# Optimization experiments

Measured on AMD Instinct MI355X. Metric: run time of the kernel, lower is better.

Reference implementation:

```python
import jax, jax.numpy as jnp
import numpy as np
import math

B, S, D, DFF, L, H, V = 8, 1024, 768, 3072, 6, 12, 70
DH = D // H


def setup_inputs():
    key = jax.random.key(0)
    ks = jax.random.split(key, 16)
    s = 0.02
    n = lambda k, sh: jax.random.normal(k, sh, dtype=jnp.float32) * s
    return {
        "x": jax.random.randint(ks[0], (B, S), 0, V),
        "mask": jnp.ones((S, S), dtype=jnp.int32),
        "color_W": n(ks[1], (4, 256)),
        "shape_W": n(ks[2], (4, 256)),
        "qty_W": n(ks[3], (4, 256)),
        "special_W": n(ks[4], (6, D)),
        "Wq": n(ks[5], (L, D, D)),
        "Wk": n(ks[6], (L, D, D)),
        "Wv": n(ks[7], (L, D, D)),
        "Wo": n(ks[8], (L, D, D)),
        "bo": jnp.zeros((L, D), jnp.float32),
        "ln1_g": jnp.ones((L, D), jnp.float32),
        "ln1_b": jnp.zeros((L, D), jnp.float32),
        "ln2_g": jnp.ones((L, D), jnp.float32),
        "ln2_b": jnp.zeros((L, D), jnp.float32),
        "W1": n(ks[9], (L, D, DFF)),
        "b1": jnp.zeros((L, DFF), jnp.float32),
        "W2": n(ks[10], (L, DFF, D)),
        "b2": jnp.zeros((L, D), jnp.float32),
        "Wout": n(ks[11], (D, V)),
        "bout": jnp.zeros((V,), jnp.float32),
    }


def _layernorm(x, g, b, eps=1e-5):
    m = x.mean(-1, keepdims=True)
    v = ((x - m) ** 2).mean(-1, keepdims=True)
    return (x - m) / jnp.sqrt(v + eps) * g + b


def _embed(x, color_W, shape_W, qty_W, special_W):
    # feature tokens (<64): color=t//16, shape=(t%16)//4, quantity=t%4
    color = jnp.clip(x // 16, 0, 3)
    shp = (x % 16) // 4
    qty = x % 4
    feat = jnp.concatenate([color_W[color], shape_W[shp], qty_W[qty]], axis=-1)  # [B,S,D]
    spec = special_W[jnp.clip(x - 64, 0, 5)]  # [B,S,D]
    emb = jnp.where((x < 64)[..., None], feat, spec)
    # sinusoidal PE: pe[p,2i]=sin(p/10000^(2i/D)), pe[p,2i+1]=cos(same angle)
    pos = jnp.arange(S, dtype=jnp.float32)[:, None]
    i = jnp.arange(0, D, 2, dtype=jnp.float32)
    ang = pos / jnp.power(10000.0, i / D)  # [S, D/2]
    pe = jnp.zeros((S, D), jnp.float32).at[:, 0::2].set(jnp.sin(ang)).at[:, 1::2].set(jnp.cos(ang))
    return emb * math.sqrt(D) + pe


def reference(x, mask, color_W, shape_W, qty_W, special_W, Wq, Wk, Wv, Wo, bo,
              ln1_g, ln1_b, ln2_g, ln2_b, W1, b1, W2, b2, Wout, bout):
    h = _embed(x, color_W, shape_W, qty_W, special_W)  # [B,S,D]
    neg_mask = (mask == 0)[None, None]  # [1,1,S,S]
    for l in range(L):
        q = (h @ Wq[l]).reshape(B, S, H, DH).transpose(0, 2, 1, 3)
        k = (h @ Wk[l]).reshape(B, S, H, DH).transpose(0, 2, 1, 3)
        v = (h @ Wv[l]).reshape(B, S, H, DH).transpose(0, 2, 1, 3)
        scores = jnp.einsum('bhqd,bhkd->bhqk', q, k) / math.sqrt(DH)
        scores = jnp.where(neg_mask, -1e9, scores)
        w = jax.nn.softmax(scores, axis=-1)
        o = jnp.einsum('bhqk,bhkd->bhqd', w, v).transpose(0, 2, 1, 3).reshape(B, S, D)
        o = o @ Wo[l] + bo[l]
        h = _layernorm(h + o, ln1_g[l], ln1_b[l])
        f = jax.nn.relu(h @ W1[l] + b1[l]) @ W2[l] + b2[l]
        h = _layernorm(h + f, ln2_g[l], ln2_b[l])
    return h @ Wout + bout  # [B,S,V]
```

## Files before the change

kernel.cpp:

```cpp
#include <hip/hip_runtime.h>
#include <hip/hip_bf16.h>

#define B_   8
#define S_   1024
#define D_   768
#define DFF_ 3072
#define L_   6
#define H_   12
#define DH_  64
#define V_   70
#define M_   (B_*S_)

typedef __attribute__((ext_vector_type(4))) float  f32x4;
typedef __attribute__((ext_vector_type(8))) short  s16x8;
typedef __attribute__((ext_vector_type(8))) __bf16 bfv8;
typedef __hip_bfloat16 bf16;

__device__ __forceinline__ float b2f(short u) {
  return __uint_as_float(((unsigned)(unsigned short)u) << 16);
}

__device__ __forceinline__ f32x4 mfma16x16x32(s16x8 a, s16x8 b, f32x4 c) {
  return __builtin_amdgcn_mfma_f32_16x16x32_bf16(
      __builtin_bit_cast(bfv8, a), __builtin_bit_cast(bfv8, b), c, 0, 0, 0);
}

__global__ __launch_bounds__(256)
void embed_kernel(const int* __restrict__ x,
                  const float* __restrict__ cW, const float* __restrict__ sW,
                  const float* __restrict__ qW, const float* __restrict__ spW,
                  float* __restrict__ hf, bf16* __restrict__ hb)
{
  int tok  = blockIdx.x;
  int spos = tok & (S_ - 1);
  int t    = x[tok];
  for (int idx = threadIdx.x; idx < D_; idx += 256) {
    float e;
    if (t < 64) {
      int color = t >> 4;       if (color > 3) color = 3;
      int shp   = (t & 15) >> 2;
      int qty   = t & 3;
      e = (idx < 256) ? cW[color*256 + idx]
        : (idx < 512) ? sW[shp*256 + idx - 256]
                      : qW[qty*256 + idx - 512];
    } else {
      int sp = t - 64; if (sp > 5) sp = 5;
      e = spW[sp*D_ + idx];
    }
    int   i2  = idx & ~1;
    float ang = (float)spos * expf(-logf(10000.f) * (float)i2 / (float)D_);
    float pe  = (idx & 1) ? cosf(ang) : sinf(ang);
    float v   = e * 27.712812921102035f + pe;
    hf[(size_t)tok*D_ + idx] = v;
    hb[(size_t)tok*D_ + idx] = __float2bfloat16(v);
  }
}

__global__ __launch_bounds__(256)
void transpose_kernel(const float* __restrict__ in, bf16* __restrict__ out,
                      int K, int N)
{
  __shared__ __align__(16) float s[64][65];
  int n0 = blockIdx.x * 64, k0 = blockIdx.y * 64;
  int tx = threadIdx.x & 63, ty = threadIdx.x >> 6;
  #pragma unroll
  for (int i = 0; i < 16; i++) {
    int r = i*4 + ty;
    s[r][tx] = in[(size_t)(k0 + r)*N + n0 + tx];
  }
  __syncthreads();
  #pragma unroll
  for (int i = 0; i < 16; i++) {
    int r = i*4 + ty;
    out[(size_t)(n0 + r)*K + k0 + tx] = __float2bfloat16(s[tx][r]);
  }
}

__global__ __launch_bounds__(256)
void vT_kernel(const bf16* __restrict__ v, bf16* __restrict__ vt)
{
  __shared__ short tile[64][68];
  int b = blockIdx.z, h = blockIdx.y, s0 = blockIdx.x*64;
  int tr = threadIdx.x >> 4, tc4 = (threadIdx.x & 15)*4;
  #pragma unroll
  for (int i = 0; i < 4; i++) {
    int row = i*16 + tr;
    short4 w = *(const short4*)((const short*)v + (size_t)(b*S_ + s0 + row)*D_ + h*DH_ + tc4);
    tile[row][tc4+0]=w.x; tile[row][tc4+1]=w.y; tile[row][tc4+2]=w.z; tile[row][tc4+3]=w.w;
  }
  __syncthreads();
  #pragma unroll
  for (int i = 0; i < 4; i++) {
    int d = i*16 + tr;
    short4 o2;
    o2.x = tile[tc4+0][d]; o2.y = tile[tc4+1][d]; o2.z = tile[tc4+2][d]; o2.w = tile[tc4+3][d];
    *(short4*)((short*)vt + ((size_t)(b*H_ + h)*DH_ + d)*S_ + s0 + tc4) = o2;
  }
}

__global__ __launch_bounds__(256)
void maskb_kernel(const int* __restrict__ mask, bf16* __restrict__ mb)
{
  int i = (blockIdx.x*256 + threadIdx.x)*4;
  int4 mv = *(const int4*)(mask + i);
  bf16 z = __float2bfloat16(0.f), ng = __float2bfloat16(-1e9f);
  mb[i+0] = mv.x ? z : ng;
  mb[i+1] = mv.y ? z : ng;
  mb[i+2] = mv.z ? z : ng;
  mb[i+3] = mv.w ? z : ng;
}

template<bool BIAS, bool RELU, bool OUTBF16>
__global__ __launch_bounds__(256, 2)
void gemm_kernel(const bf16* __restrict__ A, const bf16* __restrict__ BT,
                 const float* __restrict__ bias,
                 float* __restrict__ Cf, bf16* __restrict__ Cb,
                 int N, int K)
{
  __shared__ __align__(16) short As[4][128][8];
  __shared__ __align__(16) short Bs[4][128][8];
  int t = threadIdx.x;
  int wave = t >> 6, lane = t & 63;
  int wr = wave >> 1, wc = wave & 1;
  int brow = blockIdx.x * 128, bcol = blockIdx.y * 128;
  int r0 = t & 127, kc = t >> 7;
  const short* Ap = (const short*)A + (size_t)(brow + r0)*K + kc*8;
  const short* Bp = (const short*)BT + (size_t)(bcol + r0)*K + kc*8;
  int lr = lane & 15, kg = lane >> 4;

  f32x4 acc[4][4] = {};
  s16x8 a0 = *(const s16x8*)(Ap);
  s16x8 a1 = *(const s16x8*)(Ap + 16);
  s16x8 b0 = *(const s16x8*)(Bp);
  s16x8 b1 = *(const s16x8*)(Bp + 16);

  for (int kk = 0; kk < K; kk += 32) {
    __syncthreads();
    *(s16x8*)&As[kc  ][r0][0] = a0;
    *(s16x8*)&As[kc+2][r0][0] = a1;
    *(s16x8*)&Bs[kc  ][r0][0] = b0;
    *(s16x8*)&Bs[kc+2][r0][0] = b1;
    __syncthreads();
    if (kk + 32 < K) {
      a0 = *(const s16x8*)(Ap + kk + 32);
      a1 = *(const s16x8*)(Ap + kk + 48);
      b0 = *(const s16x8*)(Bp + kk + 32);
      b1 = *(const s16x8*)(Bp + kk + 48);
    }
    s16x8 af[4], bq[4];
    #pragma unroll
    for (int m = 0; m < 4; m++) af[m] = *(const s16x8*)&As[kg][wr*64 + m*16 + lr][0];
    #pragma unroll
    for (int n = 0; n < 4; n++) bq[n] = *(const s16x8*)&Bs[kg][wc*64 + n*16 + lr][0];
    #pragma unroll
    for (int m = 0; m < 4; m++)
      #pragma unroll
      for (int n = 0; n < 4; n++)
        acc[m][n] = mfma16x16x32(af[m], bq[n], acc[m][n]);
  }

  int lg = lane >> 4;
  #pragma unroll
  for (int n = 0; n < 4; n++) {
    int col = bcol + wc*64 + n*16 + lr;
    float bv = 0.f;
    if (BIAS) bv = bias[col];
    #pragma unroll
    for (int m = 0; m < 4; m++) {
      int row0 = brow + wr*64 + m*16 + lg*4;
      #pragma unroll
      for (int r = 0; r < 4; r++) {
        float v = acc[m][n][r] + bv;
        if (RELU) v = fmaxf(v, 0.f);
        size_t off = (size_t)(row0 + r)*N + col;
        if (OUTBF16) Cb[off] = __float2bfloat16(v);
        else         Cf[off] = v;
      }
    }
  }
}

__global__ __launch_bounds__(256)
void fattn_kernel(const bf16* __restrict__ Q, const bf16* __restrict__ K,
                  const bf16* __restrict__ Vt, const bf16* __restrict__ Mb,
                  bf16* __restrict__ O)
{
  __shared__ __align__(16) bf16 p_lds[4][16][72];
  int b = blockIdx.z, h = blockIdx.y;
  int wave = threadIdx.x >> 6, lane = threadIdx.x & 63;
  int c = lane & 15, g = lane >> 4;
  int q0 = blockIdx.x*64 + wave*16;

  const short* Qp = (const short*)Q + (size_t)(b*S_ + q0 + c)*D_ + h*DH_;
  s16x8 qf0 = *(const s16x8*)(Qp + g*8);
  s16x8 qf1 = *(const s16x8*)(Qp + 32 + g*8);
  const short* Kb = (const short*)K + (size_t)(b*S_)*D_ + h*DH_;
  const short* Vb = (const short*)Vt + (size_t)(b*H_ + h)*DH_*S_;
  const short* Mp = (const short*)Mb + (size_t)(q0 + g*4)*S_;

  f32x4 o[4] = {};
  float m[4]  = {-3.0e38f, -3.0e38f, -3.0e38f, -3.0e38f};
  float l[4]  = {0.f, 0.f, 0.f, 0.f};

  for (int k0 = 0; k0 < S_; k0 += 64) {
    f32x4 s[4];
    #pragma unroll
    for (int n = 0; n < 4; n++) {
      const short* kp = Kb + (size_t)(k0 + n*16 + c)*D_;
      s16x8 kf0 = *(const s16x8*)(kp + g*8);
      s16x8 kf1 = *(const s16x8*)(kp + 32 + g*8);
      f32x4 z = {};
      z    = mfma16x16x32(qf0, kf0, z);
      s[n] = mfma16x16x32(qf1, kf1, z);
    }
    #pragma unroll
    for (int n = 0; n < 4; n++)
      #pragma unroll
      for (int r = 0; r < 4; r++)
        s[n][r] = s[n][r]*0.125f + b2f(Mp[(size_t)r*S_ + k0 + n*16 + c]);

    float tm[4];
    #pragma unroll
    for (int r = 0; r < 4; r++)
      tm[r] = fmaxf(fmaxf(s[0][r], s[1][r]), fmaxf(s[2][r], s[3][r]));
    #pragma unroll
    for (int off = 1; off < 16; off <<= 1)
      #pragma unroll
      for (int r = 0; r < 4; r++)
        tm[r] = fmaxf(tm[r], __shfl_xor(tm[r], off));

    float al[4];
    #pragma unroll
    for (int r = 0; r < 4; r++) {
      float mn = fmaxf(m[r], tm[r]);
      al[r] = __expf(m[r] - mn);
      m[r] = mn;
    }
    f32x4 p[4];
    float rs[4] = {0.f, 0.f, 0.f, 0.f};
    #pragma unroll
    for (int n = 0; n < 4; n++)
      #pragma unroll
      for (int r = 0; r < 4; r++) {
        float pv = __expf(s[n][r] - m[r]);
        p[n][r] = pv; rs[r] += pv;
      }
    #pragma unroll
    for (int r = 0; r < 4; r++) l[r] = l[r]*al[r] + rs[r];
    #pragma unroll
    for (int n = 0; n < 4; n++)
      #pragma unroll
      for (int r = 0; r < 4; r++) o[n][r] *= al[r];

    #pragma unroll
    for (int n = 0; n < 4; n++)
      #pragma unroll
      for (int r = 0; r < 4; r++)
        p_lds[wave][g*4 + r][n*16 + c] = __float2bfloat16(p[n][r]);
    s16x8 pa0 = *(const s16x8*)&p_lds[wave][c][g*8];
    s16x8 pa1 = *(const s16x8*)&p_lds[wave][c][32 + g*8];

    #pragma unroll
    for (int n = 0; n < 4; n++) {
      const short* vp = Vb + (size_t)(n*16 + c)*S_ + k0;
      s16x8 vf0 = *(const s16x8*)(vp + g*8);
      s16x8 vf1 = *(const s16x8*)(vp + 32 + g*8);
      o[n] = mfma16x16x32(pa0, vf0, o[n]);
      o[n] = mfma16x16x32(pa1, vf1, o[n]);
    }
  }

  #pragma unroll
  for (int off = 1; off < 16; off <<= 1)
    #pragma unroll
    for (int r = 0; r < 4; r++) l[r] += __shfl_xor(l[r], off);

  bf16* Op = O + (size_t)(b*S_ + q0 + g*4)*D_ + h*DH_;
  #pragma unroll
  for (int r = 0; r < 4; r++) {
    float inv = 1.f / l[r];
    #pragma unroll
    for (int n = 0; n < 4; n++)
      Op[(size_t)r*D_ + n*16 + c] = __float2bfloat16(o[n][r] * inv);
  }
}

__global__ __launch_bounds__(256)
void ln_kernel(float* h, const float* __restrict__ delta,
               const float* __restrict__ g, const float* __restrict__ bta,
               bf16* __restrict__ hb)
{
  int row = blockIdx.x;
  float* rp = h + (size_t)row*D_;
  const float* dp = delta + (size_t)row*D_;
  int t = threadIdx.x;
  float v[3];
  float sum = 0.f, sq = 0.f;
  #pragma unroll
  for (int i = 0; i < 3; i++) {
    float xv = rp[t + i*256] + dp[t + i*256];
    v[i] = xv; sum += xv; sq += xv*xv;
  }
  #pragma unroll
  for (int o = 1; o < 64; o <<= 1) { sum += __shfl_xor(sum, o); sq += __shfl_xor(sq, o); }
  __shared__ float ws[8];
  int wave = t >> 6, lane = t & 63;
  if (lane == 0) { ws[wave] = sum; ws[wave+4] = sq; }
  __syncthreads();
  sum = ws[0]+ws[1]+ws[2]+ws[3];
  sq  = ws[4]+ws[5]+ws[6]+ws[7];
  float m   = sum * (1.f/768.f);
  float var = sq * (1.f/768.f) - m*m;
  float rs  = rsqrtf(var + 1e-5f);
  #pragma unroll
  for (int i = 0; i < 3; i++) {
    int idx = t + i*256;
    float y = (v[i] - m) * rs * g[idx] + bta[idx];
    rp[idx] = y;
    hb[(size_t)row*D_ + idx] = __float2bfloat16(y);
  }
}

__global__ __launch_bounds__(128)
void final_kernel(const float* __restrict__ h, const float* __restrict__ Wout,
                  const float* __restrict__ bout, float* __restrict__ out)
{
  __shared__ float hs[D_];
  int row = blockIdx.x;
  for (int i = threadIdx.x; i < D_; i += 128) hs[i] = h[(size_t)row*D_ + i];
  __syncthreads();
  int n = threadIdx.x;
  if (n < V_) {
    float acc = bout[n];
    for (int d = 0; d < D_; d++) acc += hs[d] * Wout[d*V_ + n];
    out[(size_t)row*V_ + n] = acc;
  }
}

extern "C" void kernel_launch(void* const* d_in, const int* in_sizes, int n_in,
                              void* d_out, int out_size, void* d_ws, size_t ws_size,
                              hipStream_t stream)
{
  (void)in_sizes; (void)n_in; (void)out_size; (void)ws_size;
  const int*   x    = (const int*)d_in[0];
  const int*   mask = (const int*)d_in[1];
  const float* cW   = (const float*)d_in[2];
  const float* sW   = (const float*)d_in[3];
  const float* qW   = (const float*)d_in[4];
  const float* spW  = (const float*)d_in[5];
  const float* Wq   = (const float*)d_in[6];
  const float* Wk   = (const float*)d_in[7];
  const float* Wv   = (const float*)d_in[8];
  const float* Wo   = (const float*)d_in[9];
  const float* bo   = (const float*)d_in[10];
  const float* ln1g = (const float*)d_in[11];
  const float* ln1b = (const float*)d_in[12];
  const float* ln2g = (const float*)d_in[13];
  const float* ln2b = (const float*)d_in[14];
  const float* W1   = (const float*)d_in[15];
  const float* b1   = (const float*)d_in[16];
  const float* W2   = (const float*)d_in[17];
  const float* b2   = (const float*)d_in[18];
  const float* Wout = (const float*)d_in[19];
  const float* bout = (const float*)d_in[20];
  float* out = (float*)d_out;

  char* p = (char*)d_ws;
  auto alloc = [&](size_t bytes) {
    char* r = p; p += (bytes + 1023) & ~(size_t)1023; return r;
  };
  float* hf     = (float*)alloc((size_t)M_*D_*4);
  float* delta  = (float*)alloc((size_t)M_*D_*4);
  bf16*  hb     = (bf16*)alloc((size_t)M_*D_*2);
  bf16*  ob     = (bf16*)alloc((size_t)M_*D_*2);
  char*  shared = alloc((size_t)M_*DFF_*2);
  bf16*  qb     = (bf16*)shared;
  bf16*  kb     = (bf16*)(shared + (size_t)M_*D_*2);
  bf16*  vb     = (bf16*)(shared + (size_t)2*M_*D_*2);
  bf16*  vt     = (bf16*)(shared + (size_t)3*M_*D_*2);
  bf16*  f1     = (bf16*)shared;
  bf16*  wqT    = (bf16*)alloc((size_t)D_*D_*2);
  bf16*  wkT    = (bf16*)alloc((size_t)D_*D_*2);
  bf16*  wvT    = (bf16*)alloc((size_t)D_*D_*2);
  bf16*  woT    = (bf16*)alloc((size_t)D_*D_*2);
  bf16*  w1T    = (bf16*)alloc((size_t)D_*DFF_*2);
  bf16*  w2T    = (bf16*)alloc((size_t)DFF_*D_*2);
  bf16*  maskb  = (bf16*)alloc((size_t)S_*S_*2);

  maskb_kernel<<<S_*S_/1024, 256, 0, stream>>>(mask, maskb);
  embed_kernel<<<M_, 256, 0, stream>>>(x, cW, sW, qW, spW, hf, hb);

  for (int l = 0; l < L_; l++) {
    transpose_kernel<<<dim3(12,12), 256, 0, stream>>>(Wq + (size_t)l*D_*D_, wqT, D_, D_);
    transpose_kernel<<<dim3(12,12), 256, 0, stream>>>(Wk + (size_t)l*D_*D_, wkT, D_, D_);
    transpose_kernel<<<dim3(12,12), 256, 0, stream>>>(Wv + (size_t)l*D_*D_, wvT, D_, D_);
    transpose_kernel<<<dim3(12,12), 256, 0, stream>>>(Wo + (size_t)l*D_*D_, woT, D_, D_);
    transpose_kernel<<<dim3(48,12), 256, 0, stream>>>(W1 + (size_t)l*D_*DFF_, w1T, D_, DFF_);
    transpose_kernel<<<dim3(12,48), 256, 0, stream>>>(W2 + (size_t)l*DFF_*D_, w2T, DFF_, D_);

    gemm_kernel<false,false,true><<<dim3(64,6), 256, 0, stream>>>(hb, wqT, nullptr, nullptr, qb, D_, D_);
    gemm_kernel<false,false,true><<<dim3(64,6), 256, 0, stream>>>(hb, wkT, nullptr, nullptr, kb, D_, D_);
    gemm_kernel<false,false,true><<<dim3(64,6), 256, 0, stream>>>(hb, wvT, nullptr, nullptr, vb, D_, D_);

    vT_kernel<<<dim3(16, H_, B_), 256, 0, stream>>>(vb, vt);
    fattn_kernel<<<dim3(S_/64, H_, B_), 256, 0, stream>>>(qb, kb, vt, maskb, ob);

    gemm_kernel<true,false,false><<<dim3(64,6), 256, 0, stream>>>(ob, woT, bo + l*D_, delta, nullptr, D_, D_);
    ln_kernel<<<M_, 256, 0, stream>>>(hf, delta, ln1g + l*D_, ln1b + l*D_, hb);

    gemm_kernel<true,true,true ><<<dim3(64,24), 256, 0, stream>>>(hb, w1T, b1 + l*DFF_, nullptr, f1, DFF_, D_);
    gemm_kernel<true,false,false><<<dim3(64,6), 256, 0, stream>>>(f1, w2T, b2 + l*D_, delta, nullptr, D_, DFF_);
    ln_kernel<<<M_, 256, 0, stream>>>(hf, delta, ln2g + l*D_, ln2b + l*D_, hb);
  }

  final_kernel<<<M_, 128, 0, stream>>>(hf, Wout, bout, out);
}
```

Before: 3.437 ms.

## Fuse QKV GEMM, use direct-to-LDS loads, skip all-ones mask tiles, widen attention blocks

```diff
diff --git a/kernel.cpp b/kernel.cpp
--- a/kernel.cpp
+++ b/kernel.cpp
@@ -10,6 +10,7 @@
 #define DH_  64
 #define V_   70
 #define M_   (B_*S_)
+#define QKVLD 2304
 
 typedef __attribute__((ext_vector_type(4))) float  f32x4;
 typedef __attribute__((ext_vector_type(8))) short  s16x8;
@@ -23,6 +24,12 @@
 __device__ __forceinline__ f32x4 mfma16x16x32(s16x8 a, s16x8 b, f32x4 c) {
   return __builtin_amdgcn_mfma_f32_16x16x32_bf16(
       __builtin_bit_cast(bfv8, a), __builtin_bit_cast(bfv8, b), c, 0, 0, 0);
+}
+
+__device__ __forceinline__ void gload16(const void* g, void* lds) {
+  __builtin_amdgcn_global_load_lds(
+      (const __attribute__((address_space(1))) unsigned int*)g,
+      (__attribute__((address_space(3))) unsigned int*)lds, 16, 0, 0);
 }
 
 __global__ __launch_bounds__(256)
@@ -77,7 +84,7 @@
 }
 
 __global__ __launch_bounds__(256)
-void vT_kernel(const bf16* __restrict__ v, bf16* __restrict__ vt)
+void vT_kernel(const bf16* __restrict__ v, int ld, bf16* __restrict__ vt)
 {
   __shared__ short tile[64][68];
   int b = blockIdx.z, h = blockIdx.y, s0 = blockIdx.x*64;
@@ -85,7 +92,7 @@
   #pragma unroll
   for (int i = 0; i < 4; i++) {
     int row = i*16 + tr;
-    short4 w = *(const short4*)((const short*)v + (size_t)(b*S_ + s0 + row)*D_ + h*DH_ + tc4);
+    short4 w = *(const short4*)((const short*)v + (size_t)(b*S_ + s0 + row)*ld + h*DH_ + tc4);
     tile[row][tc4+0]=w.x; tile[row][tc4+1]=w.y; tile[row][tc4+2]=w.z; tile[row][tc4+3]=w.w;
   }
   __syncthreads();
@@ -108,6 +115,21 @@
   mb[i+1] = mv.y ? z : ng;
   mb[i+2] = mv.z ? z : ng;
   mb[i+3] = mv.w ? z : ng;
+}
+
+__global__ __launch_bounds__(64)
+void mflag_kernel(const int* __restrict__ mask, int* __restrict__ mf)
+{
+  int qt = blockIdx.x >> 4, kt = blockIdx.x & 15;
+  const int* row = mask + (size_t)(qt*64 + threadIdx.x)*S_ + kt*64;
+  int allv = 1;
+  #pragma unroll
+  for (int j = 0; j < 64; j += 4) {
+    int4 v = *(const int4*)(row + j);
+    allv &= (v.x && v.y && v.z && v.w) ? 1 : 0;
+  }
+  unsigned long long bal = __ballot(allv);
+  if (threadIdx.x == 0) mf[blockIdx.x] = (bal != ~0ULL) ? 1 : 0;
 }
 
 template<bool BIAS, bool RELU, bool OUTBF16>
@@ -129,24 +151,14 @@
   int lr = lane & 15, kg = lane >> 4;
 
   f32x4 acc[4][4] = {};
-  s16x8 a0 = *(const s16x8*)(Ap);
-  s16x8 a1 = *(const s16x8*)(Ap + 16);
-  s16x8 b0 = *(const s16x8*)(Bp);
-  s16x8 b1 = *(const s16x8*)(Bp + 16);
 
   for (int kk = 0; kk < K; kk += 32) {
     __syncthreads();
-    *(s16x8*)&As[kc  ][r0][0] = a0;
-    *(s16x8*)&As[kc+2][r0][0] = a1;
-    *(s16x8*)&Bs[kc  ][r0][0] = b0;
-    *(s16x8*)&Bs[kc+2][r0][0] = b1;
+    gload16(Ap + kk,      &As[kc  ][r0][0]);
+    gload16(Ap + kk + 16, &As[kc+2][r0][0]);
+    gload16(Bp + kk,      &Bs[kc  ][r0][0]);
+    gload16(Bp + kk + 16, &Bs[kc+2][r0][0]);
     __syncthreads();
-    if (kk + 32 < K) {
-      a0 = *(const s16x8*)(Ap + kk + 32);
-      a1 = *(const s16x8*)(Ap + kk + 48);
-      b0 = *(const s16x8*)(Bp + kk + 32);
-      b1 = *(const s16x8*)(Bp + kk + 48);
-    }
     s16x8 af[4], bq[4];
     #pragma unroll
     for (int m = 0; m < 4; m++) af[m] = *(const s16x8*)&As[kg][wr*64 + m*16 + lr][0];
@@ -181,107 +193,143 @@
 }
 
 __global__ __launch_bounds__(256)
-void fattn_kernel(const bf16* __restrict__ Q, const bf16* __restrict__ K,
-                  const bf16* __restrict__ Vt, const bf16* __restrict__ Mb,
+void fattn_kernel(const bf16* __restrict__ QKV, const bf16* __restrict__ Vt,
+                  const bf16* __restrict__ Mb, const int* __restrict__ MF,
                   bf16* __restrict__ O)
 {
-  __shared__ __align__(16) bf16 p_lds[4][16][72];
+  __shared__ __align__(16) bf16 p_lds[4][32][72];
   int b = blockIdx.z, h = blockIdx.y;
   int wave = threadIdx.x >> 6, lane = threadIdx.x & 63;
   int c = lane & 15, g = lane >> 4;
-  int q0 = blockIdx.x*64 + wave*16;
-
-  const short* Qp = (const short*)Q + (size_t)(b*S_ + q0 + c)*D_ + h*DH_;
-  s16x8 qf0 = *(const s16x8*)(Qp + g*8);
-  s16x8 qf1 = *(const s16x8*)(Qp + 32 + g*8);
-  const short* Kb = (const short*)K + (size_t)(b*S_)*D_ + h*DH_;
+  int q0 = blockIdx.x*128 + wave*32;
+
+  s16x8 qf[2][2];
+  #pragma unroll
+  for (int u = 0; u < 2; u++) {
+    const short* Qp = (const short*)QKV + (size_t)(b*S_ + q0 + u*16 + c)*QKVLD + h*DH_;
+    qf[u][0] = *(const s16x8*)(Qp + g*8);
+    qf[u][1] = *(const s16x8*)(Qp + 32 + g*8);
+  }
+  const short* Kb = (const short*)QKV + (size_t)(b*S_)*QKVLD + D_ + h*DH_;
   const short* Vb = (const short*)Vt + (size_t)(b*H_ + h)*DH_*S_;
   const short* Mp = (const short*)Mb + (size_t)(q0 + g*4)*S_;
-
-  f32x4 o[4] = {};
-  float m[4]  = {-3.0e38f, -3.0e38f, -3.0e38f, -3.0e38f};
-  float l[4]  = {0.f, 0.f, 0.f, 0.f};
-
-  for (int k0 = 0; k0 < S_; k0 += 64) {
-    f32x4 s[4];
+  const int*   MFq = MF + (q0 >> 6)*16;
+
+  f32x4 o[2][4] = {};
+  float m[2][4], l[2][4];
+  #pragma unroll
+  for (int u = 0; u < 2; u++)
+    #pragma unroll
+    for (int r = 0; r < 4; r++) { m[u][r] = -3.0e38f; l[u][r] = 0.f; }
+
+  for (int kt = 0; kt < 16; kt++) {
+    int k0 = kt*64;
+    f32x4 s[2][4];
     #pragma unroll
     for (int n = 0; n < 4; n++) {
-      const short* kp = Kb + (size_t)(k0 + n*16 + c)*D_;
+      const short* kp = Kb + (size_t)(k0 + n*16 + c)*QKVLD;
       s16x8 kf0 = *(const s16x8*)(kp + g*8);
       s16x8 kf1 = *(const s16x8*)(kp + 32 + g*8);
-      f32x4 z = {};
-      z    = mfma16x16x32(qf0, kf0, z);
-      s[n] = mfma16x16x32(qf1, kf1, z);
-    }
-    #pragma unroll
-    for (int n = 0; n < 4; n++)
+      #pragma unroll
+      for (int u = 0; u < 2; u++) {
+        f32x4 z = {};
+        z       = mfma16x16x32(qf[u][0], kf0, z);
+        s[u][n] = mfma16x16x32(qf[u][1], kf1, z);
+      }
+    }
+    if (MFq[kt]) {
+      #pragma unroll
+      for (int u = 0; u < 2; u++)
+        #pragma unroll
+        for (int n = 0; n < 4; n++)
+          #pragma unroll
+          for (int r = 0; r < 4; r++)
+            s[u][n][r] = s[u][n][r]*0.125f
+                       + b2f(Mp[(size_t)(u*16 + r)*S_ + k0 + n*16 + c]);
+    } else {
+      #pragma unroll
+      for (int u = 0; u < 2; u++)
+        #pragma unroll
+        for (int n = 0; n < 4; n++)
+          #pragma unroll
+          for (int r = 0; r < 4; r++)
+            s[u][n][r] *= 0.125f;
+    }
+
+    #pragma unroll
+    for (int u = 0; u < 2; u++) {
+      float tm[4];
       #pragma unroll
       for (int r = 0; r < 4; r++)
-        s[n][r] = s[n][r]*0.125f + b2f(Mp[(size_t)r*S_ + k0 + n*16 + c]);
-
-    float tm[4];
-    #pragma unroll
-    for (int r = 0; r < 4; r++)
-      tm[r] = fmaxf(fmaxf(s[0][r], s[1][r]), fmaxf(s[2][r], s[3][r]));
-    #pragma unroll
-    for (int off = 1; off < 16; off <<= 1)
-      #pragma unroll
-      for (int r = 0; r < 4; r++)
-        tm[r] = fmaxf(tm[r], __shfl_xor(tm[r], off));
-
-    float al[4];
-    #pragma unroll
-    for (int r = 0; r < 4; r++) {
-      float mn = fmaxf(m[r], tm[r]);
-      al[r] = __expf(m[r] - mn);
-      m[r] = mn;
-    }
-    f32x4 p[4];
-    float rs[4] = {0.f, 0.f, 0.f, 0.f};
-    #pragma unroll
-    for (int n = 0; n < 4; n++)
+        tm[r] = fmaxf(fmaxf(s[u][0][r], s[u][1][r]), fmaxf(s[u][2][r], s[u][3][r]));
+      #pragma unroll
+      for (int off = 1; off < 16; off <<= 1)
+        #pragma unroll
+        for (int r = 0; r < 4; r++)
+          tm[r] = fmaxf(tm[r], __shfl_xor(tm[r], off));
+
+      float al[4];
       #pragma unroll
       for (int r = 0; r < 4; r++) {
-        float pv = __expf(s[n][r] - m[r]);
-        p[n][r] = pv; rs[r] += pv;
+        float mn = fmaxf(m[u][r], tm[r]);
+        al[r] = __expf(m[u][r] - mn);
+        m[u][r] = mn;
       }
-    #pragma unroll
-    for (int r = 0; r < 4; r++) l[r] = l[r]*al[r] + rs[r];
-    #pragma unroll
-    for (int n = 0; n < 4; n++)
-      #pragma unroll
-      for (int r = 0; r < 4; r++) o[n][r] *= al[r];
-
-    #pragma unroll
-    for (int n = 0; n < 4; n++)
-      #pragma unroll
-      for (int r = 0; r < 4; r++)
-        p_lds[wave][g*4 + r][n*16 + c] = __float2bfloat16(p[n][r]);
-    s16x8 pa0 = *(const s16x8*)&p_lds[wave][c][g*8];
-    s16x8 pa1 = *(const s16x8*)&p_lds[wave][c][32 + g*8];
-
+      f32x4 p[4];
+      float rs[4] = {0.f, 0.f, 0.f, 0.f};
+      #pragma unroll
+      for (int n = 0; n < 4; n++)
+        #pragma unroll
+        for (int r = 0; r < 4; r++) {
+          float pv = __expf(s[u][n][r] - m[u][r]);
+          p[n][r] = pv; rs[r] += pv;
+        }
+      #pragma unroll
+      for (int r = 0; r < 4; r++) l[u][r] = l[u][r]*al[r] + rs[r];
+      #pragma unroll
+      for (int n = 0; n < 4; n++)
+        #pragma unroll
+        for (int r = 0; r < 4; r++) o[u][n][r] *= al[r];
+      #pragma unroll
+      for (int n = 0; n < 4; n++)
+        #pragma unroll
+        for (int r = 0; r < 4; r++)
+          p_lds[wave][u*16 + g*4 + r][n*16 + c] = __float2bfloat16(p[n][r]);
+    }
+
+    s16x8 pa[2][2];
+    #pragma unroll
+    for (int u = 0; u < 2; u++) {
+      pa[u][0] = *(const s16x8*)&p_lds[wave][u*16 + c][g*8];
+      pa[u][1] = *(const s16x8*)&p_lds[wave][u*16 + c][32 + g*8];
+    }
     #pragma unroll
     for (int n = 0; n < 4; n++) {
       const short* vp = Vb + (size_t)(n*16 + c)*S_ + k0;
       s16x8 vf0 = *(const s16x8*)(vp + g*8);
       s16x8 vf1 = *(const s16x8*)(vp + 32 + g*8);
-      o[n] = mfma16x16x32(pa0, vf0, o[n]);
-      o[n] = mfma16x16x32(pa1, vf1, o[n]);
-    }
-  }
-
-  #pragma unroll
-  for (int off = 1; off < 16; off <<= 1)
-    #pragma unroll
-    for (int r = 0; r < 4; r++) l[r] += __shfl_xor(l[r], off);
-
-  bf16* Op = O + (size_t)(b*S_ + q0 + g*4)*D_ + h*DH_;
-  #pragma unroll
-  for (int r = 0; r < 4; r++) {
-    float inv = 1.f / l[r];
-    #pragma unroll
-    for (int n = 0; n < 4; n++)
-      Op[(size_t)r*D_ + n*16 + c] = __float2bfloat16(o[n][r] * inv);
+      #pragma unroll
+      for (int u = 0; u < 2; u++) {
+        o[u][n] = mfma16x16x32(pa[u][0], vf0, o[u][n]);
+        o[u][n] = mfma16x16x32(pa[u][1], vf1, o[u][n]);
+      }
+    }
+  }
+
+  #pragma unroll
+  for (int u = 0; u < 2; u++) {
+    #pragma unroll
+    for (int off = 1; off < 16; off <<= 1)
+      #pragma unroll
+      for (int r = 0; r < 4; r++) l[u][r] += __shfl_xor(l[u][r], off);
+    bf16* Op = O + (size_t)(b*S_ + q0 + u*16 + g*4)*D_ + h*DH_;
+    #pragma unroll
+    for (int r = 0; r < 4; r++) {
+      float inv = 1.f / l[u][r];
+      #pragma unroll
+      for (int n = 0; n < 4; n++)
+        Op[(size_t)r*D_ + n*16 + c] = __float2bfloat16(o[u][n][r] * inv);
+    }
   }
 }
 
@@ -374,36 +422,32 @@
   bf16*  hb     = (bf16*)alloc((size_t)M_*D_*2);
   bf16*  ob     = (bf16*)alloc((size_t)M_*D_*2);
   char*  shared = alloc((size_t)M_*DFF_*2);
-  bf16*  qb     = (bf16*)shared;
-  bf16*  kb     = (bf16*)(shared + (size_t)M_*D_*2);
-  bf16*  vb     = (bf16*)(shared + (size_t)2*M_*D_*2);
-  bf16*  vt     = (bf16*)(shared + (size_t)3*M_*D_*2);
+  bf16*  qkv    = (bf16*)shared;
+  bf16*  vt     = (bf16*)(shared + (size_t)M_*QKVLD*2);
   bf16*  f1     = (bf16*)shared;
-  bf16*  wqT    = (bf16*)alloc((size_t)D_*D_*2);
-  bf16*  wkT    = (bf16*)alloc((size_t)D_*D_*2);
-  bf16*  wvT    = (bf16*)alloc((size_t)D_*D_*2);
+  bf16*  wqkvT  = (bf16*)alloc((size_t)QKVLD*D_*2);
   bf16*  woT    = (bf16*)alloc((size_t)D_*D_*2);
   bf16*  w1T    = (bf16*)alloc((size_t)D_*DFF_*2);
   bf16*  w2T    = (bf16*)alloc((size_t)DFF_*D_*2);
   bf16*  maskb  = (bf16*)alloc((size_t)S_*S_*2);
+  int*   mflag  = (int*)alloc(256*4);
 
   maskb_kernel<<<S_*S_/1024, 256, 0, stream>>>(mask, maskb);
+  mflag_kernel<<<256, 64, 0, stream>>>(mask, mflag);
   embed_kernel<<<M_, 256, 0, stream>>>(x, cW, sW, qW, spW, hf, hb);
 
   for (int l = 0; l < L_; l++) {
-    transpose_kernel<<<dim3(12,12), 256, 0, stream>>>(Wq + (size_t)l*D_*D_, wqT, D_, D_);
-    transpose_kernel<<<dim3(12,12), 256, 0, stream>>>(Wk + (size_t)l*D_*D_, wkT, D_, D_);
-    transpose_kernel<<<dim3(12,12), 256, 0, stream>>>(Wv + (size_t)l*D_*D_, wvT, D_, D_);
+    transpose_kernel<<<dim3(12,12), 256, 0, stream>>>(Wq + (size_t)l*D_*D_, wqkvT, D_, D_);
+    transpose_kernel<<<dim3(12,12), 256, 0, stream>>>(Wk + (size_t)l*D_*D_, wqkvT + (size_t)D_*D_, D_, D_);
+    transpose_kernel<<<dim3(12,12), 256, 0, stream>>>(Wv + (size_t)l*D_*D_, wqkvT + (size_t)2*D_*D_, D_, D_);
     transpose_kernel<<<dim3(12,12), 256, 0, stream>>>(Wo + (size_t)l*D_*D_, woT, D_, D_);
     transpose_kernel<<<dim3(48,12), 256, 0, stream>>>(W1 + (size_t)l*D_*DFF_, w1T, D_, DFF_);
     transpose_kernel<<<dim3(12,48), 256, 0, stream>>>(W2 + (size_t)l*DFF_*D_, w2T, DFF_, D_);
 
-    gemm_kernel<false,false,true><<<dim3(64,6), 256, 0, stream>>>(hb, wqT, nullptr, nullptr, qb, D_, D_);
-    gemm_kernel<false,false,true><<<dim3(64,6), 256, 0, stream>>>(hb, wkT, nullptr, nullptr, kb, D_, D_);
-    gemm_kernel<false,false,true><<<dim3(64,6), 256, 0, stream>>>(hb, wvT, nullptr, nullptr, vb, D_, D_);
-
-    vT_kernel<<<dim3(16, H_, B_), 256, 0, stream>>>(vb, vt);
-    fattn_kernel<<<dim3(S_/64, H_, B_), 256, 0, stream>>>(qb, kb, vt, maskb, ob);
+    gemm_kernel<false,false,true><<<dim3(64,18), 256, 0, stream>>>(hb, wqkvT, nullptr, nullptr, qkv, QKVLD, D_);
+
+    vT_kernel<<<dim3(16, H_, B_), 256, 0, stream>>>(qkv + 2*D_, QKVLD, vt);
+    fattn_kernel<<<dim3(S_/128, H_, B_), 256, 0, stream>>>(qkv, vt, maskb, mflag, ob);
 
     gemm_kernel<true,false,false><<<dim3(64,6), 256, 0, stream>>>(ob, woT, bo + l*D_, delta, nullptr, D_, D_);
     ln_kernel<<<M_, 256, 0, stream>>>(hf, delta, ln1g + l*D_, ln1b + l*D_, hb);
```

Result: faster. 3.206 ms (-6.7%).
